# Kernel tuning notes

Hardware: AMD Instinct MI355X
Metric: run time of the kernel (lower is better)

The kernel has to match this reference:

```python
import jax, jax.numpy as jnp
import numpy as np
from jax import lax

B, M, N = 4096, 306, 984
LAMBDA = 0.1
MAX_ITER = 50


def setup_inputs() -> dict:
    key = jax.random.key(0)
    k1, k2, k3, k4 = jax.random.split(key, 4)
    return {
        "r_real": jax.random.normal(k1, (B, M), dtype=jnp.float32),
        "r_imag": jax.random.normal(k2, (B, M), dtype=jnp.float32),
        # phi buffer: torch.randn(M, N, dtype=complex64) -> real/imag each ~N(0, 1/2)?
        # torch.randn(complex64) draws real & imag each from N(0, 1/sqrt(2)^2)=N(0,0.5).
        "phi_real": jax.random.normal(k3, (M, N), dtype=jnp.float32) * np.float32(1.0 / np.sqrt(2.0)),
        "phi_imag": jax.random.normal(k4, (M, N), dtype=jnp.float32) * np.float32(1.0 / np.sqrt(2.0)),
    }


def reference(r_real, r_imag, phi_real, phi_imag):
    phi = (phi_real + 1j * phi_imag).astype(jnp.complex64)          # [M, N]
    r = (r_real + 1j * r_imag).astype(jnp.complex64)                # [B, M]
    # step_size = 1 / ||phi||_2^2  (spectral norm squared)
    step = (1.0 / jnp.linalg.norm(phi, ord=2) ** 2).real.astype(jnp.float32)
    thresh = (LAMBDA * step).astype(jnp.float32)
    phi_c = jnp.conj(phi)

    def body(w, _):
        # error = w @ phi.T - r : [B, M]
        error = jnp.einsum("bn,mn->bm", w, phi) - r
        # gradient = error @ conj(phi) : [B, N]
        grad = jnp.einsum("bm,mn->bn", error, phi_c)
        w_next = w - step * grad
        w_mag = jnp.abs(w_next)
        new_mag = jax.nn.relu(w_mag - thresh)
        # polar(new_mag, angle(w_next))
        w_new = (new_mag * jnp.exp(1j * jnp.angle(w_next))).astype(jnp.complex64)
        return w_new, None

    w0 = jnp.zeros((r.shape[0], N), dtype=jnp.complex64)
    w, _ = lax.scan(body, w0, None, length=MAX_ITER)
    return jnp.abs(w).astype(jnp.float32)
```

## Files before the change

kernel.cpp:

```cpp
#include <hip/hip_runtime.h>
#include <math.h>

#define Bb 4096
#define Mm 306
#define Nn 984
#define NCP 1024
#define KA 2048
#define ITERS 50
#define KSQ 9

typedef _Float16 f16x8 __attribute__((ext_vector_type(8)));
typedef float f32x16 __attribute__((ext_vector_type(16)));

__device__ __forceinline__ void cmac(float2& c, const float2 a, const float2 b) {
    c.x = fmaf(a.x, b.x, c.x);
    c.x = fmaf(-a.y, b.y, c.x);
    c.y = fmaf(a.x, b.y, c.y);
    c.y = fmaf(a.y, b.x, c.y);
}

__device__ __forceinline__ unsigned short f16bits(float v) {
    union { _Float16 h; unsigned short u; } cv;
    cv.h = (_Float16)v;
    return cv.u;
}
__device__ __forceinline__ float f16lo(unsigned int u) {
    union { unsigned short s; _Float16 h; } cv; cv.s = (unsigned short)(u & 0xffffu);
    return (float)cv.h;
}
__device__ __forceinline__ float f16hi(unsigned int u) {
    union { unsigned short s; _Float16 h; } cv; cv.s = (unsigned short)(u >> 16);
    return (float)cv.h;
}

__device__ __forceinline__ void load_lds16(const void* g, void* l) {
    __builtin_amdgcn_global_load_lds((const __attribute__((address_space(1))) void*)g,
                                     (__attribute__((address_space(3))) void*)l, 16, 0, 0);
}

__device__ __forceinline__ size_t swzA(int b, int c) {
    return ((size_t)(((b >> 7) * 32 + (c >> 5)) * 1024 + ((c >> 2) & 7) * 128 + (b & 127))) * 4 + (c & 3);
}
__device__ __forceinline__ size_t swzB(int jr, int q) {
    return ((size_t)(((jr >> 7) * 32 + (q >> 5)) * 1024 + ((q >> 2) & 7) * 128 + (jr & 127))) * 4 + (q & 3);
}
__device__ __forceinline__ size_t swzA2(int b, int c) {
    return ((size_t)(((b >> 7) * 10 + (c >> 5)) * 1024 + ((c >> 2) & 7) * 128 + (b & 127))) * 4 + (c & 3);
}
__device__ __forceinline__ size_t swzB2(int jr, int q) {
    return ((size_t)(((jr >> 7) * 10 + (q >> 5)) * 1024 + ((q >> 2) & 7) * 128 + (jr & 127))) * 4 + (q & 3);
}

__global__ void gram_kernel(const float* __restrict__ pr, const float* __restrict__ pi,
                            float2* __restrict__ G) {
    __shared__ float2 As[32][33];
    __shared__ float2 Bs[32][33];
    int tx = threadIdx.x, ty = threadIdx.y;
    int t = ty * 16 + tx;
    int i0 = blockIdx.y * 32, j0 = blockIdx.x * 32;
    int zs = blockIdx.z * 246;
    int ze = zs + 246 < Nn ? zs + 246 : Nn;
    float2 acc[2][2] = {};
    for (int k0 = zs; k0 < ze; k0 += 32) {
        #pragma unroll
        for (int rep = 0; rep < 4; ++rep) {
            int idx = t + rep * 256;
            int rr = idx >> 5, cc = idx & 31;
            int gk = k0 + cc;
            int gi = i0 + rr, gj = j0 + rr;
            float2 a = make_float2(0.f, 0.f), b = make_float2(0.f, 0.f);
            if (gk < ze) {
                if (gi < Mm) a = make_float2(pr[(size_t)gi * Nn + gk], pi[(size_t)gi * Nn + gk]);
                if (gj < Mm) b = make_float2(pr[(size_t)gj * Nn + gk], pi[(size_t)gj * Nn + gk]);
            }
            As[rr][cc] = a; Bs[rr][cc] = b;
        }
        __syncthreads();
        #pragma unroll 8
        for (int kk = 0; kk < 32; ++kk) {
            float2 a0 = As[ty * 2][kk], a1 = As[ty * 2 + 1][kk];
            float2 b0 = Bs[tx * 2][kk], b1 = Bs[tx * 2 + 1][kk];
            #define GMAC(qq, aa, bb) \
                qq.x = fmaf(aa.x, bb.x, qq.x); qq.x = fmaf(aa.y, bb.y, qq.x); \
                qq.y = fmaf(aa.y, bb.x, qq.y); qq.y = fmaf(-aa.x, bb.y, qq.y);
            GMAC(acc[0][0], a0, b0) GMAC(acc[0][1], a0, b1)
            GMAC(acc[1][0], a1, b0) GMAC(acc[1][1], a1, b1)
            #undef GMAC
        }
        __syncthreads();
    }
    #pragma unroll
    for (int i = 0; i < 2; ++i) {
        int gi = i0 + ty * 2 + i;
        #pragma unroll
        for (int j = 0; j < 2; ++j) {
            int gj = j0 + tx * 2 + j;
            if (gi < Mm && gj < Mm) {
                atomicAdd(&G[gi * Mm + gj].x, acc[i][j].x);
                atomicAdd(&G[gi * Mm + gj].y, acc[i][j].y);
            }
        }
    }
}

__global__ void frobz_kernel(const float2* __restrict__ H, float* __restrict__ slot,
                             float2* __restrict__ dst, int n) {
    int idx = blockIdx.x * blockDim.x + threadIdx.x;
    int stride = gridDim.x * blockDim.x;
    float s = 0.f;
    for (int i = idx; i < n; i += stride) {
        float2 v = H[i];
        s = fmaf(v.x, v.x, s);
        s = fmaf(v.y, v.y, s);
        dst[i] = make_float2(0.f, 0.f);
    }
    #pragma unroll
    for (int o = 32; o > 0; o >>= 1) s += __shfl_down(s, o, 64);
    __shared__ float wsum[4];
    int lane = threadIdx.x & 63, wv = threadIdx.x >> 6;
    if (lane == 0) wsum[wv] = s;
    __syncthreads();
    if (threadIdx.x == 0) atomicAdd(slot, wsum[0] + wsum[1] + wsum[2] + wsum[3]);
}

__global__ void sqmm_kernel(const float2* __restrict__ A, float2* __restrict__ C,
                            const float* __restrict__ fslot) {
    __shared__ float2 As[32][33];
    __shared__ float2 Bs[32][33];
    float inv = 1.0f / fslot[0];
    int tx = threadIdx.x, ty = threadIdx.y;
    int t = ty * 16 + tx;
    int r0 = blockIdx.y * 32, c0 = blockIdx.x * 32;
    int zs = blockIdx.z * 80;
    int ze = zs + 80 < Mm ? zs + 80 : Mm;
    float2 acc[2][2] = {};
    for (int k0 = zs; k0 < ze; k0 += 32) {
        #pragma unroll
        for (int i = 0; i < 4; ++i) {
            int idx = t + i * 256;
            int rr = idx >> 5, cc = idx & 31;
            int gr = r0 + rr, gk = k0 + cc;
            As[rr][cc] = (gr < Mm && gk < ze) ? A[gr * Mm + gk] : make_float2(0.f, 0.f);
            int gk2 = k0 + rr, gc = c0 + cc;
            Bs[rr][cc] = (gk2 < ze && gc < Mm) ? A[gk2 * Mm + gc] : make_float2(0.f, 0.f);
        }
        __syncthreads();
        #pragma unroll 8
        for (int kk = 0; kk < 32; ++kk) {
            float2 a0 = As[ty * 2][kk], a1 = As[ty * 2 + 1][kk];
            float2 b0 = Bs[kk][tx * 2], b1 = Bs[kk][tx * 2 + 1];
            cmac(acc[0][0], a0, b0); cmac(acc[0][1], a0, b1);
            cmac(acc[1][0], a1, b0); cmac(acc[1][1], a1, b1);
        }
        __syncthreads();
    }
    #pragma unroll
    for (int i = 0; i < 2; ++i) {
        int gr = r0 + ty * 2 + i;
        #pragma unroll
        for (int j = 0; j < 2; ++j) {
            int gc = c0 + tx * 2 + j;
            if (gr < Mm && gc < Mm) {
                atomicAdd(&C[gr * Mm + gc].x, acc[i][j].x * inv);
                atomicAdd(&C[gr * Mm + gc].y, acc[i][j].y * inv);
            }
        }
    }
}

__global__ void ray1_kernel(const float2* __restrict__ H, float2* __restrict__ v) {
    int t = blockIdx.x;
    int k = threadIdx.x;
    float sx = 0.f, sy = 0.f;
    for (int j = k; j < Mm; j += 256) {
        float2 h = H[(size_t)t * Mm + j];
        sx += h.x; sy += h.y;
    }
    #pragma unroll
    for (int o = 32; o > 0; o >>= 1) { sx += __shfl_down(sx, o, 64); sy += __shfl_down(sy, o, 64); }
    __shared__ float wx[4], wy[4];
    int lane = k & 63, wv = k >> 6;
    if (lane == 0) { wx[wv] = sx; wy[wv] = sy; }
    __syncthreads();
    if (k == 0) v[t] = make_float2(wx[0] + wx[1] + wx[2] + wx[3],
                                   wy[0] + wy[1] + wy[2] + wy[3]);
}

__global__ void ray2_kernel(const float2* __restrict__ G, const float2* __restrict__ v,
                            float* __restrict__ slots) {
    int t = blockIdx.x;
    int k0 = threadIdx.x;
    float ux = 0.f, uy = 0.f;
    for (int k = k0; k < Mm; k += 256) {
        float2 g = G[(size_t)k * Mm + t];
        float2 vk = v[k];
        ux = fmaf(g.x, vk.x, ux); ux = fmaf(g.y, vk.y, ux);
        uy = fmaf(g.x, vk.y, uy); uy = fmaf(-g.y, vk.x, uy);
    }
    #pragma unroll
    for (int o = 32; o > 0; o >>= 1) { ux += __shfl_down(ux, o, 64); uy += __shfl_down(uy, o, 64); }
    __shared__ float wx[4], wy[4];
    int lane = k0 & 63, wv = k0 >> 6;
    if (lane == 0) { wx[wv] = ux; wy[wv] = uy; }
    __syncthreads();
    if (k0 == 0) {
        float sux = wx[0] + wx[1] + wx[2] + wx[3];
        float suy = wy[0] + wy[1] + wy[2] + wy[3];
        float2 vt = v[t];
        atomicAdd(&slots[16], vt.x * sux + vt.y * suy);
        atomicAdd(&slots[17], vt.x * vt.x + vt.y * vt.y);
    }
}

__global__ void ray3_kernel(const float* __restrict__ slots, float* __restrict__ sc) {
    float step = slots[17] / slots[16];
    sc[0] = step;
    sc[1] = 0.1f * step;
}

__global__ void qpack_kernel(const float* __restrict__ pr, const float* __restrict__ pi,
                             unsigned int* __restrict__ Bu, const float* __restrict__ sc) {
    __shared__ float2 Pn[16][33];
    __shared__ float2 Pc[16][65];
    float nstep = -sc[0];
    int t = threadIdx.x;
    int tx = t & 15, ty = t >> 4;
    int n0 = blockIdx.x * 32, c0 = blockIdx.y * 64;
    float2 q[2][4] = {};
    for (int m0 = 0; m0 < Mm; m0 += 16) {
        #pragma unroll
        for (int rep = 0; rep < 6; ++rep) {
            int idx = t + rep * 256;
            if (idx < 512) {
                int mm = idx >> 5, col = idx & 31;
                int gm = m0 + mm;
                float2 a = make_float2(0.f, 0.f);
                if (gm < Mm && n0 + col < Nn)
                    a = make_float2(pr[(size_t)gm * Nn + n0 + col], pi[(size_t)gm * Nn + n0 + col]);
                Pn[mm][col] = a;
            } else {
                int idx2 = idx - 512;
                int mm = idx2 >> 6, col = idx2 & 63;
                int gm = m0 + mm;
                float2 b = make_float2(0.f, 0.f);
                if (gm < Mm && c0 + col < Nn)
                    b = make_float2(pr[(size_t)gm * Nn + c0 + col], pi[(size_t)gm * Nn + c0 + col]);
                Pc[mm][col] = b;
            }
        }
        __syncthreads();
        #pragma unroll
        for (int mm = 0; mm < 16; ++mm) {
            float2 a0 = Pn[mm][ty * 2], a1 = Pn[mm][ty * 2 + 1];
            float2 b0 = Pc[mm][tx], b1 = Pc[mm][16 + tx];
            float2 b2 = Pc[mm][32 + tx], b3 = Pc[mm][48 + tx];
            #define QMAC(qq, aa, bb) \
                qq.x = fmaf(aa.x, bb.x, qq.x); qq.x = fmaf(aa.y, bb.y, qq.x); \
                qq.y = fmaf(aa.y, bb.x, qq.y); qq.y = fmaf(-aa.x, bb.y, qq.y);
            QMAC(q[0][0], a0, b0) QMAC(q[0][1], a0, b1) QMAC(q[0][2], a0, b2) QMAC(q[0][3], a0, b3)
            QMAC(q[1][0], a1, b0) QMAC(q[1][1], a1, b1) QMAC(q[1][2], a1, b2) QMAC(q[1][3], a1, b3)
            #undef QMAC
        }
        __syncthreads();
    }
    #pragma unroll
    for (int i = 0; i < 2; ++i) {
        int n = n0 + ty * 2 + i;
        #pragma unroll
        for (int j = 0; j < 4; ++j) {
            int c = c0 + j * 16 + tx;
            if (n < Nn && c < Nn) {
                float MR = fmaf(nstep, q[i][j].x, (n == c) ? 1.0f : 0.0f);
                float MI = nstep * q[i][j].y;
                unsigned short hR = f16bits(MR);
                unsigned short hI = f16bits(MI);
                unsigned short nhI = hI ^ 0x8000u;
                int jr = ((c >> 5) * 64) + (c & 31);
                Bu[swzB(jr, n)]      = (unsigned)hR | ((unsigned)nhI << 16);
                Bu[swzB(jr + 32, n)] = (unsigned)hI | ((unsigned)hR << 16);
            }
        }
    }
}

__global__ void rpack_kernel(const float* __restrict__ rr, const float* __restrict__ ri,
                             unsigned int* __restrict__ rp16) {
    int b = blockIdx.x * 256 + threadIdx.x;
    int m = blockIdx.y;
    rp16[swzA2(b, m)] = (unsigned)f16bits(rr[(size_t)b * Mm + m]) |
                        ((unsigned)f16bits(ri[(size_t)b * Mm + m]) << 16);
}

__global__ void ppack2_kernel(const float* __restrict__ pr, const float* __restrict__ pi,
                              unsigned int* __restrict__ B2u, const float* __restrict__ sc) {
    int n = blockIdx.x * 256 + threadIdx.x;
    int m = blockIdx.y;
    if (n >= Nn) return;
    float s = sc[0];
    float xr = pr[(size_t)m * Nn + n], xi = pi[(size_t)m * Nn + n];
    unsigned short x = f16bits(-s * xr), y = f16bits(-s * xi);
    int jr2 = ((n >> 5) * 64) + (n & 31);
    B2u[swzB2(jr2, m)]      = (unsigned)x | ((unsigned)y << 16);
    B2u[swzB2(jr2 + 32, m)] = (unsigned)(y ^ 0x8000u) | ((unsigned)x << 16);
}

__global__ __launch_bounds__(256, 2) void rphi_mfma_kernel(
    const _Float16* __restrict__ rp16, const _Float16* __restrict__ B2,
    unsigned int* __restrict__ rph16) {
    __shared__ _Float16 As[8192];
    __shared__ _Float16 Bs[8192];
    int tid = threadIdx.x;
    int lane = tid & 63, wv = tid >> 6;
    int wm = wv & 1, wn = wv >> 1;
    int bblk = blockIdx.x, nblk = blockIdx.y;
    int l31 = lane & 31, lh = lane >> 5;

    f32x16 acc[2][2] = {};

    for (int kt = 0; kt < 10; ++kt) {
        #pragma unroll
        for (int c = 0; c < 4; ++c) {
            int u = c * 256 + tid;
            const char* ga = (const char*)rp16 + (((size_t)(bblk * 10 + kt)) * 1024 + u) * 16;
            load_lds16(ga, &As[(size_t)(c * 256 + wv * 64) * 8]);
            const char* gb = (const char*)B2 + (((size_t)(nblk * 10 + kt)) * 1024 + u) * 16;
            load_lds16(gb, &Bs[(size_t)(c * 256 + wv * 64) * 8]);
        }
        __syncthreads();
        #pragma unroll
        for (int s = 0; s < 4; ++s) {
            int kq = s * 2 + lh;
            f16x8 af[2], bfr[2];
            #pragma unroll
            for (int mt = 0; mt < 2; ++mt)
                af[mt] = *reinterpret_cast<const f16x8*>(
                    &As[(size_t)(kq * 128 + wm * 64 + mt * 32 + l31) * 8]);
            #pragma unroll
            for (int nt = 0; nt < 2; ++nt)
                bfr[nt] = *reinterpret_cast<const f16x8*>(
                    &Bs[(size_t)(kq * 128 + wn * 64 + nt * 32 + l31) * 8]);
            #pragma unroll
            for (int mt = 0; mt < 2; ++mt)
                #pragma unroll
                for (int nt = 0; nt < 2; ++nt)
                    acc[mt][nt] = __builtin_amdgcn_mfma_f32_32x32x16_f16(af[mt], bfr[nt], acc[mt][nt], 0, 0, 0);
        }
        __syncthreads();
    }

    int b0 = bblk * 128;
    int c = nblk * 64 + wn * 32 + l31;
    #pragma unroll
    for (int mt = 0; mt < 2; ++mt) {
        #pragma unroll
        for (int reg = 0; reg < 16; ++reg) {
            int row = b0 + wm * 64 + mt * 32 + ((reg & 3) + 8 * (reg >> 2) + 4 * lh);
            rph16[(size_t)row * NCP + c] =
                (unsigned)f16bits(-acc[mt][0][reg]) | ((unsigned)f16bits(-acc[mt][1][reg]) << 16);
        }
    }
}

__global__ __launch_bounds__(512) void ista9_kernel(
    const _Float16* __restrict__ wfi, const _Float16* __restrict__ Bq,
    unsigned int* __restrict__ wfo,
    const unsigned int* __restrict__ rph16,
    const float* __restrict__ sc, float* __restrict__ out, int last) {
    __shared__ _Float16 As0[8192], As1[8192];
    __shared__ _Float16 Bs0[2][8192], Bs1[2][8192];
    int tid = threadIdx.x;
    int lane = tid & 63, wv = tid >> 6;
    int wm = wv >> 2, wn = wv & 3;
    int id = blockIdx.x;
    int x = id & 7;
    int n = id >> 3;
    int bblk = (x & 3) * 8 + (n & 7);
    int nb2  = (x >> 2) * 4 + (n >> 3);
    int l31 = lane & 31, lh = lane >> 5;
    int slab = wn >> 1, chg = wn & 1;

    f32x16 acc[2][2] = {};

    const char* gA  = (const char*)wfi + (size_t)bblk * 32 * 1024 * 16;
    const char* gB0 = (const char*)Bq + (size_t)(nb2 * 2 + 0) * 32 * 1024 * 16;
    const char* gB1 = (const char*)Bq + (size_t)(nb2 * 2 + 1) * 32 * 1024 * 16;

    #define STAGE9(kt, Ad, Bd)                                                        \
        {                                                                             \
            _Float16* Ap = (Ad);                                                      \
            _Float16* Bp0 = &(Bd)[0][0];                                              \
            _Float16* Bp1 = &(Bd)[1][0];                                              \
            _Pragma("unroll")                                                         \
            for (int cc = 0; cc < 2; ++cc) {                                          \
                int u = cc * 512 + tid;                                               \
                size_t ldst = (size_t)(cc * 512 + wv * 64) * 8;                       \
                load_lds16(gA + ((size_t)(kt) * 1024 + u) * 16, &Ap[ldst]);           \
                load_lds16(gB0 + ((size_t)(kt) * 1024 + u) * 16, &Bp0[ldst]);         \
                load_lds16(gB1 + ((size_t)(kt) * 1024 + u) * 16, &Bp1[ldst]);         \
            }                                                                         \
        }

    #define COMPUTE9(Asrc, Bsrc)                                                      \
        {                                                                             \
            _Pragma("unroll")                                                         \
            for (int s = 0; s < 4; ++s) {                                             \
                int kq = s * 2 + lh;                                                  \
                f16x8 af[2], bf[2];                                                   \
                _Pragma("unroll")                                                     \
                for (int mt = 0; mt < 2; ++mt)                                        \
                    af[mt] = *reinterpret_cast<const f16x8*>(                         \
                        &(Asrc)[(size_t)(kq * 128 + wm * 64 + mt * 32 + l31) * 8]);   \
                _Pragma("unroll")                                                     \
                for (int nt = 0; nt < 2; ++nt)                                        \
                    bf[nt] = *reinterpret_cast<const f16x8*>(                         \
                        &(Bsrc)[slab][(size_t)(kq * 128 + chg * 64 + nt * 32 + l31) * 8]); \
                _Pragma("unroll")                                                     \
                for (int mt = 0; mt < 2; ++mt)                                        \
                    _Pragma("unroll")                                                 \
                    for (int nt = 0; nt < 2; ++nt)                                    \
                        acc[mt][nt] = __builtin_amdgcn_mfma_f32_32x32x16_f16(         \
                            af[mt], bf[nt], acc[mt][nt], 0, 0, 0);                    \
            }                                                                         \
        }

    STAGE9(0, As0, Bs0);
    for (int kt = 0; kt < 30; kt += 2) {
        STAGE9(kt + 1, As1, Bs1);
        asm volatile("s_waitcnt vmcnt(6)" ::: "memory");
        __builtin_amdgcn_s_barrier();
        COMPUTE9(As0, Bs0);
        __builtin_amdgcn_s_barrier();
        STAGE9(kt + 2, As0, Bs0);
        asm volatile("s_waitcnt vmcnt(6)" ::: "memory");
        __builtin_amdgcn_s_barrier();
        COMPUTE9(As1, Bs1);
        __builtin_amdgcn_s_barrier();
    }
    asm volatile("s_waitcnt vmcnt(0)" ::: "memory");
    __builtin_amdgcn_s_barrier();
    COMPUTE9(As0, Bs0);
    #undef STAGE9
    #undef COMPUTE9

    float thr = sc[1];
    int b0 = bblk * 128;
    int c = nb2 * 128 + wn * 32 + l31;
    #pragma unroll
    for (int mt = 0; mt < 2; ++mt) {
        #pragma unroll
        for (int reg = 0; reg < 16; ++reg) {
            int row = b0 + wm * 64 + mt * 32 + ((reg & 3) + 8 * (reg >> 2) + 4 * lh);
            unsigned int ru = rph16[(size_t)row * NCP + c];
            float zr = acc[mt][0][reg] + f16lo(ru);
            float zi = acc[mt][1][reg] + f16hi(ru);
            float mag = sqrtf(zr * zr + zi * zi);
            float nm = mag - thr;
            float f = (nm > 0.f) ? (nm / mag) : 0.f;
            wfo[swzA(row, c)] = (unsigned)f16bits(zr * f) | ((unsigned)f16bits(zi * f) << 16);
            if (last && c < Nn) out[(size_t)row * Nn + c] = fmaxf(nm, 0.f);
        }
    }
}

extern "C" void kernel_launch(void* const* d_in, const int* in_sizes, int n_in,
                              void* d_out, int out_size, void* d_ws, size_t ws_size,
                              hipStream_t stream) {
    const float* rr = (const float*)d_in[0];
    const float* ri = (const float*)d_in[1];
    const float* pr = (const float*)d_in[2];
    const float* pi = (const float*)d_in[3];
    float* out = (float*)d_out;

    char* ws = (char*)d_ws;
    size_t off = 0;
    _Float16* wf0 = (_Float16*)(ws + off); off += (size_t)Bb * KA * sizeof(_Float16);
    _Float16* wf1 = (_Float16*)(ws + off); off += (size_t)Bb * KA * sizeof(_Float16);
    _Float16* Bq  = (_Float16*)(ws + off); off += (size_t)2048 * 2048 * sizeof(_Float16);
    unsigned int* rph16 = (unsigned int*)(ws + off); off += (size_t)Bb * NCP * 4;
    _Float16* rp16 = (_Float16*)(ws + off); off += (size_t)Bb * 640 * sizeof(_Float16);
    _Float16* B2  = (_Float16*)(ws + off); off += (size_t)2048 * 640 * sizeof(_Float16);
    float2* G = (float2*)(ws + off);     off += (size_t)Mm * Mm * sizeof(float2);
    float2* H1 = (float2*)(ws + off);    off += (size_t)Mm * Mm * sizeof(float2);
    float2* H2 = (float2*)(ws + off);    off += (size_t)Mm * Mm * sizeof(float2);
    float2* vvec = (float2*)(ws + off);  off += (size_t)Mm * sizeof(float2);
    float* slots = (float*)(ws + off);   off += 64 * sizeof(float);
    float* sc = slots + 32;

    (void)hipMemsetAsync(wf0, 0, (size_t)Bb * KA * sizeof(_Float16), stream);
    (void)hipMemsetAsync(Bq, 0, (size_t)2048 * 2048 * sizeof(_Float16), stream);
    (void)hipMemsetAsync(rp16, 0, (size_t)Bb * 640 * sizeof(_Float16), stream);
    (void)hipMemsetAsync(B2, 0, (size_t)2048 * 640 * sizeof(_Float16), stream);
    (void)hipMemsetAsync(slots, 0, 64 * sizeof(float), stream);
    (void)hipMemsetAsync(G, 0, (size_t)Mm * Mm * sizeof(float2), stream);

    gram_kernel<<<dim3(10, 10, 4), dim3(16, 16), 0, stream>>>(pr, pi, G);
    float2* bufs[2] = { H1, H2 };
    const float2* src = G;
    for (int s = 0; s < KSQ; ++s) {
        float2* dst = bufs[s & 1];
        frobz_kernel<<<128, 256, 0, stream>>>(src, slots + s, dst, Mm * Mm);
        sqmm_kernel<<<dim3(10, 10, 4), dim3(16, 16), 0, stream>>>(src, dst, slots + s);
        src = dst;
    }
    ray1_kernel<<<Mm, 256, 0, stream>>>(src, vvec);
    ray2_kernel<<<Mm, 256, 0, stream>>>(G, vvec, slots);
    ray3_kernel<<<1, 1, 0, stream>>>(slots, sc);

    qpack_kernel<<<dim3(31, 16), 256, 0, stream>>>(pr, pi, (unsigned int*)Bq, sc);
    rpack_kernel<<<dim3(16, Mm), 256, 0, stream>>>(rr, ri, (unsigned int*)rp16);
    ppack2_kernel<<<dim3(4, Mm), 256, 0, stream>>>(pr, pi, (unsigned int*)B2, sc);
    rphi_mfma_kernel<<<dim3(32, 16), 256, 0, stream>>>(rp16, B2, rph16);

    _Float16* wbuf[2] = { wf0, wf1 };
    for (int it = 0; it < ITERS; ++it) {
        ista9_kernel<<<256, 512, 0, stream>>>(
            wbuf[it & 1], Bq, (unsigned int*)wbuf[(it + 1) & 1], rph16, sc, out,
            it == ITERS - 1 ? 1 : 0);
    }
}
```

Before: 2.817 ms.

## Halve ISTA block to 256 threads, single-buffer LDS, double per-wave tile

Replaces the 512-thread double-buffered ISTA GEMM kernel with a 256-thread kernel using a single LDS buffer. Each wave now computes a 64x64 complex tile, eight accumulators instead of four. Launch bounds now allow two blocks per CU, so cross-block occupancy can hide memory latency in place of explicit prefetch. The risk is that the loss of load/compute overlap within a block and the extra accumulator registers cost more than that occupancy gains.

```diff
diff --git a/kernel.cpp b/kernel.cpp
--- a/kernel.cpp
+++ b/kernel.cpp
@@ -361,103 +361,84 @@
     }
 }
 
-__global__ __launch_bounds__(512) void ista9_kernel(
+__global__ __launch_bounds__(256, 2) void ista11_kernel(
     const _Float16* __restrict__ wfi, const _Float16* __restrict__ Bq,
     unsigned int* __restrict__ wfo,
     const unsigned int* __restrict__ rph16,
     const float* __restrict__ sc, float* __restrict__ out, int last) {
-    __shared__ _Float16 As0[8192], As1[8192];
-    __shared__ _Float16 Bs0[2][8192], Bs1[2][8192];
+    __shared__ _Float16 As[8192];
+    __shared__ _Float16 Bs[2][8192];
     int tid = threadIdx.x;
     int lane = tid & 63, wv = tid >> 6;
-    int wm = wv >> 2, wn = wv & 3;
+    int wm = wv & 1, wn = wv >> 1;
     int id = blockIdx.x;
     int x = id & 7;
     int n = id >> 3;
     int bblk = (x & 3) * 8 + (n & 7);
     int nb2  = (x >> 2) * 4 + (n >> 3);
     int l31 = lane & 31, lh = lane >> 5;
-    int slab = wn >> 1, chg = wn & 1;
-
-    f32x16 acc[2][2] = {};
+
+    f32x16 acc[2][2][2] = {};
 
     const char* gA  = (const char*)wfi + (size_t)bblk * 32 * 1024 * 16;
     const char* gB0 = (const char*)Bq + (size_t)(nb2 * 2 + 0) * 32 * 1024 * 16;
     const char* gB1 = (const char*)Bq + (size_t)(nb2 * 2 + 1) * 32 * 1024 * 16;
 
-    #define STAGE9(kt, Ad, Bd)                                                        \
-        {                                                                             \
-            _Float16* Ap = (Ad);                                                      \
-            _Float16* Bp0 = &(Bd)[0][0];                                              \
-            _Float16* Bp1 = &(Bd)[1][0];                                              \
-            _Pragma("unroll")                                                         \
-            for (int cc = 0; cc < 2; ++cc) {                                          \
-                int u = cc * 512 + tid;                                               \
-                size_t ldst = (size_t)(cc * 512 + wv * 64) * 8;                       \
-                load_lds16(gA + ((size_t)(kt) * 1024 + u) * 16, &Ap[ldst]);           \
-                load_lds16(gB0 + ((size_t)(kt) * 1024 + u) * 16, &Bp0[ldst]);         \
-                load_lds16(gB1 + ((size_t)(kt) * 1024 + u) * 16, &Bp1[ldst]);         \
-            }                                                                         \
-        }
-
-    #define COMPUTE9(Asrc, Bsrc)                                                      \
-        {                                                                             \
-            _Pragma("unroll")                                                         \
-            for (int s = 0; s < 4; ++s) {                                             \
-                int kq = s * 2 + lh;                                                  \
-                f16x8 af[2], bf[2];                                                   \
-                _Pragma("unroll")                                                     \
-                for (int mt = 0; mt < 2; ++mt)                                        \
-                    af[mt] = *reinterpret_cast<const f16x8*>(                         \
-                        &(Asrc)[(size_t)(kq * 128 + wm * 64 + mt * 32 + l31) * 8]);   \
-                _Pragma("unroll")                                                     \
-                for (int nt = 0; nt < 2; ++nt)                                        \
-                    bf[nt] = *reinterpret_cast<const f16x8*>(                         \
-                        &(Bsrc)[slab][(size_t)(kq * 128 + chg * 64 + nt * 32 + l31) * 8]); \
-                _Pragma("unroll")                                                     \
-                for (int mt = 0; mt < 2; ++mt)                                        \
-                    _Pragma("unroll")                                                 \
-                    for (int nt = 0; nt < 2; ++nt)                                    \
-                        acc[mt][nt] = __builtin_amdgcn_mfma_f32_32x32x16_f16(         \
-                            af[mt], bf[nt], acc[mt][nt], 0, 0, 0);                    \
-            }                                                                         \
-        }
-
-    STAGE9(0, As0, Bs0);
-    for (int kt = 0; kt < 30; kt += 2) {
-        STAGE9(kt + 1, As1, Bs1);
-        asm volatile("s_waitcnt vmcnt(6)" ::: "memory");
-        __builtin_amdgcn_s_barrier();
-        COMPUTE9(As0, Bs0);
-        __builtin_amdgcn_s_barrier();
-        STAGE9(kt + 2, As0, Bs0);
-        asm volatile("s_waitcnt vmcnt(6)" ::: "memory");
-        __builtin_amdgcn_s_barrier();
-        COMPUTE9(As1, Bs1);
-        __builtin_amdgcn_s_barrier();
-    }
-    asm volatile("s_waitcnt vmcnt(0)" ::: "memory");
-    __builtin_amdgcn_s_barrier();
-    COMPUTE9(As0, Bs0);
-    #undef STAGE9
-    #undef COMPUTE9
+    for (int kt = 0; kt < 31; ++kt) {
+        #pragma unroll
+        for (int cc = 0; cc < 4; ++cc) {
+            int u = cc * 256 + tid;
+            size_t ldst = (size_t)(cc * 256 + wv * 64) * 8;
+            load_lds16(gA + ((size_t)kt * 1024 + u) * 16, &As[ldst]);
+            load_lds16(gB0 + ((size_t)kt * 1024 + u) * 16, &Bs[0][ldst]);
+            load_lds16(gB1 + ((size_t)kt * 1024 + u) * 16, &Bs[1][ldst]);
+        }
+        __syncthreads();
+        #pragma unroll
+        for (int s = 0; s < 4; ++s) {
+            int kq = s * 2 + lh;
+            f16x8 af[2], bf[2][2];
+            #pragma unroll
+            for (int mt = 0; mt < 2; ++mt)
+                af[mt] = *reinterpret_cast<const f16x8*>(
+                    &As[(size_t)(kq * 128 + wm * 64 + mt * 32 + l31) * 8]);
+            #pragma unroll
+            for (int ct = 0; ct < 2; ++ct)
+                #pragma unroll
+                for (int nt = 0; nt < 2; ++nt)
+                    bf[ct][nt] = *reinterpret_cast<const f16x8*>(
+                        &Bs[wn][(size_t)(kq * 128 + ct * 64 + nt * 32 + l31) * 8]);
+            #pragma unroll
+            for (int mt = 0; mt < 2; ++mt)
+                #pragma unroll
+                for (int ct = 0; ct < 2; ++ct)
+                    #pragma unroll
+                    for (int nt = 0; nt < 2; ++nt)
+                        acc[mt][ct][nt] = __builtin_amdgcn_mfma_f32_32x32x16_f16(
+                            af[mt], bf[ct][nt], acc[mt][ct][nt], 0, 0, 0);
+        }
+        __syncthreads();
+    }
 
     float thr = sc[1];
     int b0 = bblk * 128;
-    int c = nb2 * 128 + wn * 32 + l31;
     #pragma unroll
     for (int mt = 0; mt < 2; ++mt) {
         #pragma unroll
-        for (int reg = 0; reg < 16; ++reg) {
-            int row = b0 + wm * 64 + mt * 32 + ((reg & 3) + 8 * (reg >> 2) + 4 * lh);
-            unsigned int ru = rph16[(size_t)row * NCP + c];
-            float zr = acc[mt][0][reg] + f16lo(ru);
-            float zi = acc[mt][1][reg] + f16hi(ru);
-            float mag = sqrtf(zr * zr + zi * zi);
-            float nm = mag - thr;
-            float f = (nm > 0.f) ? (nm / mag) : 0.f;
-            wfo[swzA(row, c)] = (unsigned)f16bits(zr * f) | ((unsigned)f16bits(zi * f) << 16);
-            if (last && c < Nn) out[(size_t)row * Nn + c] = fmaxf(nm, 0.f);
+        for (int ct = 0; ct < 2; ++ct) {
+            int c = nb2 * 128 + wn * 64 + ct * 32 + l31;
+            #pragma unroll
+            for (int reg = 0; reg < 16; ++reg) {
+                int row = b0 + wm * 64 + mt * 32 + ((reg & 3) + 8 * (reg >> 2) + 4 * lh);
+                unsigned int ru = rph16[(size_t)row * NCP + c];
+                float zr = acc[mt][ct][0][reg] + f16lo(ru);
+                float zi = acc[mt][ct][1][reg] + f16hi(ru);
+                float mag = sqrtf(zr * zr + zi * zi);
+                float nm = mag - thr;
+                float f = (nm > 0.f) ? (nm / mag) : 0.f;
+                wfo[swzA(row, c)] = (unsigned)f16bits(zr * f) | ((unsigned)f16bits(zi * f) << 16);
+                if (last && c < Nn) out[(size_t)row * Nn + c] = fmaxf(nm, 0.f);
+            }
         }
     }
 }
@@ -513,7 +494,7 @@
 
     _Float16* wbuf[2] = { wf0, wf1 };
     for (int it = 0; it < ITERS; ++it) {
-        ista9_kernel<<<256, 512, 0, stream>>>(
+        ista11_kernel<<<256, 256, 0, stream>>>(
             wbuf[it & 1], Bq, (unsigned int*)wbuf[(it + 1) & 1], rph16, sc, out,
             it == ITERS - 1 ? 1 : 0);
     }
```

Measured after the change: 3.773 ms. 1.34x slower.

## Load A operand straight from global into registers, bypassing LDS staging

Applied to the files above, without the earlier changes.

The ISTA iteration GEMM no longer stages the A tile (current w) through shared memory. Each wave now loads its A fragments from global memory directly into double-buffered register arrays, while B is still staged through LDS, and the wait counts are adjusted to match. This cuts LDS footprint and LDS traffic, and the launch bounds now request two blocks per CU. The cost is more register pressure and redundant global or L2 reads, since the four waves that share a wm row each fetch the same A data.

```diff
diff --git a/kernel.cpp b/kernel.cpp
--- a/kernel.cpp
+++ b/kernel.cpp
@@ -361,12 +361,11 @@
     }
 }
 
-__global__ __launch_bounds__(512) void ista9_kernel(
+__global__ __launch_bounds__(512, 2) void ista12_kernel(
     const _Float16* __restrict__ wfi, const _Float16* __restrict__ Bq,
     unsigned int* __restrict__ wfo,
     const unsigned int* __restrict__ rph16,
     const float* __restrict__ sc, float* __restrict__ out, int last) {
-    __shared__ _Float16 As0[8192], As1[8192];
     __shared__ _Float16 Bs0[2][8192], Bs1[2][8192];
     int tid = threadIdx.x;
     int lane = tid & 63, wv = tid >> 6;
@@ -385,31 +384,35 @@
     const char* gB0 = (const char*)Bq + (size_t)(nb2 * 2 + 0) * 32 * 1024 * 16;
     const char* gB1 = (const char*)Bq + (size_t)(nb2 * 2 + 1) * 32 * 1024 * 16;
 
-    #define STAGE9(kt, Ad, Bd)                                                        \
+    #define STAGE_B12(kt, Bd)                                                         \
         {                                                                             \
-            _Float16* Ap = (Ad);                                                      \
-            _Float16* Bp0 = &(Bd)[0][0];                                              \
-            _Float16* Bp1 = &(Bd)[1][0];                                              \
             _Pragma("unroll")                                                         \
             for (int cc = 0; cc < 2; ++cc) {                                          \
                 int u = cc * 512 + tid;                                               \
                 size_t ldst = (size_t)(cc * 512 + wv * 64) * 8;                       \
-                load_lds16(gA + ((size_t)(kt) * 1024 + u) * 16, &Ap[ldst]);           \
-                load_lds16(gB0 + ((size_t)(kt) * 1024 + u) * 16, &Bp0[ldst]);         \
-                load_lds16(gB1 + ((size_t)(kt) * 1024 + u) * 16, &Bp1[ldst]);         \
+                load_lds16(gB0 + ((size_t)(kt) * 1024 + u) * 16, &(Bd)[0][ldst]);     \
+                load_lds16(gB1 + ((size_t)(kt) * 1024 + u) * 16, &(Bd)[1][ldst]);     \
             }                                                                         \
         }
 
-    #define COMPUTE9(Asrc, Bsrc)                                                      \
+    #define LOAD_A12(kt, Areg)                                                        \
+        {                                                                             \
+            _Pragma("unroll")                                                         \
+            for (int s = 0; s < 4; ++s) {                                             \
+                _Pragma("unroll")                                                     \
+                for (int mt = 0; mt < 2; ++mt)                                        \
+                    (Areg)[s * 2 + mt] = *reinterpret_cast<const f16x8*>(             \
+                        gA + ((size_t)(kt) * 1024 +                                   \
+                              ((s * 2 + lh) * 128 + wm * 64 + mt * 32 + l31)) * 16);  \
+            }                                                                         \
+        }
+
+    #define COMPUTE12(Areg, Bsrc)                                                     \
         {                                                                             \
             _Pragma("unroll")                                                         \
             for (int s = 0; s < 4; ++s) {                                             \
                 int kq = s * 2 + lh;                                                  \
-                f16x8 af[2], bf[2];                                                   \
-                _Pragma("unroll")                                                     \
-                for (int mt = 0; mt < 2; ++mt)                                        \
-                    af[mt] = *reinterpret_cast<const f16x8*>(                         \
-                        &(Asrc)[(size_t)(kq * 128 + wm * 64 + mt * 32 + l31) * 8]);   \
+                f16x8 bf[2];                                                          \
                 _Pragma("unroll")                                                     \
                 for (int nt = 0; nt < 2; ++nt)                                        \
                     bf[nt] = *reinterpret_cast<const f16x8*>(                         \
@@ -419,28 +422,33 @@
                     _Pragma("unroll")                                                 \
                     for (int nt = 0; nt < 2; ++nt)                                    \
                         acc[mt][nt] = __builtin_amdgcn_mfma_f32_32x32x16_f16(         \
-                            af[mt], bf[nt], acc[mt][nt], 0, 0, 0);                    \
+                            (Areg)[s * 2 + mt], bf[nt], acc[mt][nt], 0, 0, 0);        \
             }                                                                         \
         }
 
-    STAGE9(0, As0, Bs0);
+    f16x8 aR0[8], aR1[8];
+    STAGE_B12(0, Bs0);
+    LOAD_A12(0, aR0);
     for (int kt = 0; kt < 30; kt += 2) {
-        STAGE9(kt + 1, As1, Bs1);
-        asm volatile("s_waitcnt vmcnt(6)" ::: "memory");
+        STAGE_B12(kt + 1, Bs1);
+        LOAD_A12(kt + 1, aR1);
+        asm volatile("s_waitcnt vmcnt(12)" ::: "memory");
         __builtin_amdgcn_s_barrier();
-        COMPUTE9(As0, Bs0);
+        COMPUTE12(aR0, Bs0);
         __builtin_amdgcn_s_barrier();
-        STAGE9(kt + 2, As0, Bs0);
-        asm volatile("s_waitcnt vmcnt(6)" ::: "memory");
+        STAGE_B12(kt + 2, Bs0);
+        LOAD_A12(kt + 2, aR0);
+        asm volatile("s_waitcnt vmcnt(12)" ::: "memory");
         __builtin_amdgcn_s_barrier();
-        COMPUTE9(As1, Bs1);
+        COMPUTE12(aR1, Bs1);
         __builtin_amdgcn_s_barrier();
     }
     asm volatile("s_waitcnt vmcnt(0)" ::: "memory");
     __builtin_amdgcn_s_barrier();
-    COMPUTE9(As0, Bs0);
-    #undef STAGE9
-    #undef COMPUTE9
+    COMPUTE12(aR0, Bs0);
+    #undef STAGE_B12
+    #undef LOAD_A12
+    #undef COMPUTE12
 
     float thr = sc[1];
     int b0 = bblk * 128;
@@ -513,7 +521,7 @@
 
     _Float16* wbuf[2] = { wf0, wf1 };
     for (int it = 0; it < ITERS; ++it) {
-        ista9_kernel<<<256, 512, 0, stream>>>(
+        ista12_kernel<<<256, 512, 0, stream>>>(
             wbuf[it & 1], Bq, (unsigned int*)wbuf[(it + 1) & 1], rph16, sc, out,
             it == ITERS - 1 ? 1 : 0);
     }
```

After: 3.046 ms. +8.1%, slower.

## Fuse ISTA iterations into one cooperative kernel and exploit Hermitian Gram symmetry

Applied to the files above, without the earlier changes.

Replaces the 50 separate ista9 launches with a single cooperative kernel that loops over the iterations and uses a grid-wide sync between them. This removes per-launch overhead and tail gaps between iterations. Separately, qpack now computes only the upper triangle of the Hermitian matrix and mirrors it with conjugated entries, skipping blocks below the diagonal. The risks are that cooperative launch needs all 256 blocks to be co-resident, and that grid.sync plus fences may cost about as much as a kernel launch boundary.

```diff
diff --git a/kernel.cpp b/kernel.cpp
--- a/kernel.cpp
+++ b/kernel.cpp
@@ -1,5 +1,8 @@
 #include <hip/hip_runtime.h>
+#include <hip/hip_cooperative_groups.h>
 #include <math.h>
+
+namespace cg = cooperative_groups;
 
 #define Bb 4096
 #define Mm 306
@@ -222,10 +225,11 @@
                              unsigned int* __restrict__ Bu, const float* __restrict__ sc) {
     __shared__ float2 Pn[16][33];
     __shared__ float2 Pc[16][65];
+    int n0 = blockIdx.x * 32, c0 = blockIdx.y * 64;
+    if (c0 + 64 <= n0) return;
     float nstep = -sc[0];
     int t = threadIdx.x;
     int tx = t & 15, ty = t >> 4;
-    int n0 = blockIdx.x * 32, c0 = blockIdx.y * 64;
     float2 q[2][4] = {};
     for (int m0 = 0; m0 < Mm; m0 += 16) {
         #pragma unroll
@@ -269,7 +273,7 @@
         #pragma unroll
         for (int j = 0; j < 4; ++j) {
             int c = c0 + j * 16 + tx;
-            if (n < Nn && c < Nn) {
+            if (n < Nn && c < Nn && c >= n) {
                 float MR = fmaf(nstep, q[i][j].x, (n == c) ? 1.0f : 0.0f);
                 float MI = nstep * q[i][j].y;
                 unsigned short hR = f16bits(MR);
@@ -278,6 +282,11 @@
                 int jr = ((c >> 5) * 64) + (c & 31);
                 Bu[swzB(jr, n)]      = (unsigned)hR | ((unsigned)nhI << 16);
                 Bu[swzB(jr + 32, n)] = (unsigned)hI | ((unsigned)hR << 16);
+                if (c > n) {
+                    int jm = ((n >> 5) * 64) + (n & 31);
+                    Bu[swzB(jm, c)]      = (unsigned)hR | ((unsigned)hI << 16);
+                    Bu[swzB(jm + 32, c)] = (unsigned)nhI | ((unsigned)hR << 16);
+                }
             }
         }
     }
@@ -361,11 +370,12 @@
     }
 }
 
-__global__ __launch_bounds__(512) void ista9_kernel(
-    const _Float16* __restrict__ wfi, const _Float16* __restrict__ Bq,
-    unsigned int* __restrict__ wfo,
+__global__ __launch_bounds__(512) void ista_coop_kernel(
+    _Float16* __restrict__ wf0, _Float16* __restrict__ wf1,
+    const _Float16* __restrict__ Bq,
     const unsigned int* __restrict__ rph16,
-    const float* __restrict__ sc, float* __restrict__ out, int last) {
+    const float* __restrict__ sc, float* __restrict__ out) {
+    cg::grid_group grid = cg::this_grid();
     __shared__ _Float16 As0[8192], As1[8192];
     __shared__ _Float16 Bs0[2][8192], Bs1[2][8192];
     int tid = threadIdx.x;
@@ -379,11 +389,11 @@
     int l31 = lane & 31, lh = lane >> 5;
     int slab = wn >> 1, chg = wn & 1;
 
-    f32x16 acc[2][2] = {};
-
-    const char* gA  = (const char*)wfi + (size_t)bblk * 32 * 1024 * 16;
     const char* gB0 = (const char*)Bq + (size_t)(nb2 * 2 + 0) * 32 * 1024 * 16;
     const char* gB1 = (const char*)Bq + (size_t)(nb2 * 2 + 1) * 32 * 1024 * 16;
+    float thr = sc[1];
+    int b0 = bblk * 128;
+    int c = nb2 * 128 + wn * 32 + l31;
 
     #define STAGE9(kt, Ad, Bd)                                                        \
         {                                                                             \
@@ -423,43 +433,53 @@
             }                                                                         \
         }
 
-    STAGE9(0, As0, Bs0);
-    for (int kt = 0; kt < 30; kt += 2) {
-        STAGE9(kt + 1, As1, Bs1);
-        asm volatile("s_waitcnt vmcnt(6)" ::: "memory");
+    for (int it = 0; it < ITERS; ++it) {
+        const _Float16* wfi = (it & 1) ? wf1 : wf0;
+        unsigned int* wfo = (unsigned int*)((it & 1) ? wf0 : wf1);
+        const char* gA = (const char*)wfi + (size_t)bblk * 32 * 1024 * 16;
+
+        f32x16 acc[2][2] = {};
+
+        STAGE9(0, As0, Bs0);
+        for (int kt = 0; kt < 30; kt += 2) {
+            STAGE9(kt + 1, As1, Bs1);
+            asm volatile("s_waitcnt vmcnt(6)" ::: "memory");
+            __builtin_amdgcn_s_barrier();
+            COMPUTE9(As0, Bs0);
+            __builtin_amdgcn_s_barrier();
+            STAGE9(kt + 2, As0, Bs0);
+            asm volatile("s_waitcnt vmcnt(6)" ::: "memory");
+            __builtin_amdgcn_s_barrier();
+            COMPUTE9(As1, Bs1);
+            __builtin_amdgcn_s_barrier();
+        }
+        asm volatile("s_waitcnt vmcnt(0)" ::: "memory");
         __builtin_amdgcn_s_barrier();
         COMPUTE9(As0, Bs0);
-        __builtin_amdgcn_s_barrier();
-        STAGE9(kt + 2, As0, Bs0);
-        asm volatile("s_waitcnt vmcnt(6)" ::: "memory");
-        __builtin_amdgcn_s_barrier();
-        COMPUTE9(As1, Bs1);
-        __builtin_amdgcn_s_barrier();
-    }
-    asm volatile("s_waitcnt vmcnt(0)" ::: "memory");
-    __builtin_amdgcn_s_barrier();
-    COMPUTE9(As0, Bs0);
+
+        int last = (it == ITERS - 1);
+        #pragma unroll
+        for (int mt = 0; mt < 2; ++mt) {
+            #pragma unroll
+            for (int reg = 0; reg < 16; ++reg) {
+                int row = b0 + wm * 64 + mt * 32 + ((reg & 3) + 8 * (reg >> 2) + 4 * lh);
+                unsigned int ru = rph16[(size_t)row * NCP + c];
+                float zr = acc[mt][0][reg] + f16lo(ru);
+                float zi = acc[mt][1][reg] + f16hi(ru);
+                float mag = sqrtf(zr * zr + zi * zi);
+                float nm = mag - thr;
+                float f = (nm > 0.f) ? (nm / mag) : 0.f;
+                wfo[swzA(row, c)] = (unsigned)f16bits(zr * f) | ((unsigned)f16bits(zi * f) << 16);
+                if (last && c < Nn) out[(size_t)row * Nn + c] = fmaxf(nm, 0.f);
+            }
+        }
+
+        __threadfence();
+        grid.sync();
+        __threadfence();
+    }
     #undef STAGE9
     #undef COMPUTE9
-
-    float thr = sc[1];
-    int b0 = bblk * 128;
-    int c = nb2 * 128 + wn * 32 + l31;
-    #pragma unroll
-    for (int mt = 0; mt < 2; ++mt) {
-        #pragma unroll
-        for (int reg = 0; reg < 16; ++reg) {
-            int row = b0 + wm * 64 + mt * 32 + ((reg & 3) + 8 * (reg >> 2) + 4 * lh);
-            unsigned int ru = rph16[(size_t)row * NCP + c];
-            float zr = acc[mt][0][reg] + f16lo(ru);
-            float zi = acc[mt][1][reg] + f16hi(ru);
-            float mag = sqrtf(zr * zr + zi * zi);
-            float nm = mag - thr;
-            float f = (nm > 0.f) ? (nm / mag) : 0.f;
-            wfo[swzA(row, c)] = (unsigned)f16bits(zr * f) | ((unsigned)f16bits(zi * f) << 16);
-            if (last && c < Nn) out[(size_t)row * Nn + c] = fmaxf(nm, 0.f);
-        }
-    }
 }
 
 extern "C" void kernel_launch(void* const* d_in, const int* in_sizes, int n_in,
@@ -511,10 +531,14 @@
     ppack2_kernel<<<dim3(4, Mm), 256, 0, stream>>>(pr, pi, (unsigned int*)B2, sc);
     rphi_mfma_kernel<<<dim3(32, 16), 256, 0, stream>>>(rp16, B2, rph16);
 
-    _Float16* wbuf[2] = { wf0, wf1 };
-    for (int it = 0; it < ITERS; ++it) {
-        ista9_kernel<<<256, 512, 0, stream>>>(
-            wbuf[it & 1], Bq, (unsigned int*)wbuf[(it + 1) & 1], rph16, sc, out,
-            it == ITERS - 1 ? 1 : 0);
-    }
-}
+    {
+        _Float16* a0 = wf0; _Float16* a1 = wf1;
+        const _Float16* bq = Bq;
+        const unsigned int* rp = rph16;
+        const float* scp = sc;
+        float* op = out;
+        void* args[] = { &a0, &a1, &bq, &rp, &scp, &op };
+        (void)hipLaunchCooperativeKernel((const void*)ista_coop_kernel,
+                                         dim3(256), dim3(512), args, 0, stream);
+    }
+}
```

Measured after the change: 8.410 ms. 199% more time.
